# Performance work log

Measured on AMD Instinct MI355X. Metric: run time of the kernel, lower is better.

## Reference

```python
import jax, jax.numpy as jnp
import numpy as np

N = 50000
E = 800000
D = 96
BN_EPS = 1e-3


def setup_inputs() -> dict:
    key = jax.random.key(0)
    ks = jax.random.split(key, 8)
    inp = {
        "x": jax.random.normal(ks[0], (N, D), dtype=jnp.float32),
        "edge_src": jax.random.randint(ks[1], (E,), 0, N, dtype=jnp.int32),
        "edge_dst": jax.random.randint(ks[2], (E,), 0, N, dtype=jnp.int32),
        "edge_w": jax.random.uniform(ks[3], (E,), dtype=jnp.float32),
        "w1": jax.random.normal(ks[4], (D, D), dtype=jnp.float32) * (1.0 / np.sqrt(D)),
        "w2": jax.random.normal(ks[5], (D, D), dtype=jnp.float32) * (1.0 / np.sqrt(D)),
        "w3": jax.random.normal(ks[6], (D, D), dtype=jnp.float32) * (1.0 / np.sqrt(D)),
    }
    for i in (1, 2, 3):
        inp[f"g{i}"] = jnp.ones((D,), jnp.float32)
        inp[f"b{i}"] = jnp.zeros((D,), jnp.float32)
        inp[f"m{i}"] = jnp.zeros((D,), jnp.float32)
        inp[f"v{i}"] = jnp.ones((D,), jnp.float32)
    return inp


def _gcn(x, w, edge_src, edge_dst, edge_w):
    # GraphConvolution: h = x @ W; out = relu(adj @ h)  (sparse COO spmm)
    h = x @ w                                        # [N, D]
    msg = edge_w[:, None] * h[edge_src]              # [E, D]
    agg = jax.ops.segment_sum(msg, edge_dst, num_segments=N)  # [N, D]
    return jax.nn.relu(agg)


def _bn(x, gamma, beta, mean, var):
    # keras BatchNormalization, inference mode, eps=1e-3
    return (x - mean) * (gamma * jax.lax.rsqrt(var + BN_EPS)) + beta


def reference(x, edge_src, edge_dst, edge_w,
              w1, w2, w3,
              g1, b1, m1, v1,
              g2, b2, m2, v2,
              g3, b3, m3, v3):
    residual = x
    h = _bn(_gcn(x, w1, edge_src, edge_dst, edge_w), g1, b1, m1, v1)
    h = _bn(_gcn(h, w2, edge_src, edge_dst, edge_w), g2, b2, m2, v2)
    h = _bn(_gcn(h, w3, edge_src, edge_dst, edge_w), g3, b3, m3, v3)
    return h + residual
```

## Files before the change

kernel.cpp:

```cpp
#include <hip/hip_runtime.h>
#include <hip/hip_fp16.h>

#define DF 96
#define BN_EPS 1e-3f
#define MAXNB 1024
#define PTILE 2048
#define HTILE 2048

template<bool FUSE_BN, bool HALF_IN, bool HALF_OUT>
__global__ __launch_bounds__(192) void gemm_bn_kernel(
    const void* __restrict__ Ain, const float* __restrict__ W,
    const float* __restrict__ g, const float* __restrict__ b,
    const float* __restrict__ m, const float* __restrict__ v,
    void* __restrict__ Cout, int N)
{
    __shared__ __half2 sWh[96 * 48];
    __shared__ float   sA[64 * 100];
    __shared__ float   sS[96], sT[96];

    const int tid  = threadIdx.x;
    const int row0 = blockIdx.x * 64;

    if (FUSE_BN && tid < 96) {
        float s = g[tid] * rsqrtf(v[tid] + BN_EPS);
        sS[tid] = s;
        sT[tid] = b[tid] - m[tid] * s;
    }
    {
        const float4* Wv = reinterpret_cast<const float4*>(W);
        #pragma unroll
        for (int i = 0; i < 12; ++i) {
            int f = tid + 192 * i;
            float4 w = Wv[f];
            sWh[2 * f]     = __floats2half2_rn(w.x, w.y);
            sWh[2 * f + 1] = __floats2half2_rn(w.z, w.w);
        }
    }
    __syncthreads();

    #pragma unroll
    for (int i = 0; i < 8; ++i) {
        int f   = tid + 192 * i;
        int row = f / 24;
        int cc  = (f % 24) * 4;
        int gr  = row0 + row;
        float4 val = make_float4(0.f, 0.f, 0.f, 0.f);
        if (gr < N) {
            if (HALF_IN) {
                const __half* Ah = (const __half*)Ain + (size_t)gr * DF + cc;
                float2 raw = *reinterpret_cast<const float2*>(Ah);
                union { float2 f2; __half2 h[2]; } u; u.f2 = raw;
                float2 lo = __half22float2(u.h[0]);
                float2 hi = __half22float2(u.h[1]);
                val = make_float4(lo.x, lo.y, hi.x, hi.y);
            } else {
                val = *reinterpret_cast<const float4*>(
                          (const float*)Ain + (size_t)gr * DF + cc);
            }
            if (FUSE_BN) {
                float* p = &val.x;
                #pragma unroll
                for (int j = 0; j < 4; ++j) {
                    float x_ = p[j];
                    x_ = x_ > 0.f ? x_ : 0.f;
                    p[j] = x_ * sS[cc + j] + sT[cc + j];
                }
            }
        }
        *reinterpret_cast<float4*>(sA + row * 100 + cc) = val;
    }
    __syncthreads();

    const int tx = tid % 24, ty = tid / 24;
    float acc[8][4];
    #pragma unroll
    for (int i = 0; i < 8; ++i)
        for (int j = 0; j < 4; ++j) acc[i][j] = 0.f;

    for (int k = 0; k < 96; ++k) {
        float2 wa = __half22float2(sWh[k * 48 + tx * 2]);
        float2 wb = __half22float2(sWh[k * 48 + tx * 2 + 1]);
        #pragma unroll
        for (int i = 0; i < 8; ++i) {
            float a = sA[(ty + 8 * i) * 100 + k];
            acc[i][0] += a * wa.x;
            acc[i][1] += a * wa.y;
            acc[i][2] += a * wb.x;
            acc[i][3] += a * wb.y;
        }
    }
    const int c0 = tx * 4;
    #pragma unroll
    for (int i = 0; i < 8; ++i) {
        int gr = row0 + ty + 8 * i;
        if (gr >= N) continue;
        if (HALF_OUT) {
            __half* C = (__half*)Cout;
            ushort4 u;
            u.x = __half_as_ushort(__float2half_rn(acc[i][0]));
            u.y = __half_as_ushort(__float2half_rn(acc[i][1]));
            u.z = __half_as_ushort(__float2half_rn(acc[i][2]));
            u.w = __half_as_ushort(__float2half_rn(acc[i][3]));
            *reinterpret_cast<ushort4*>(C + (size_t)gr * DF + c0) = u;
        } else {
            float* C = (float*)Cout;
            *reinterpret_cast<float4*>(C + (size_t)gr * DF + c0) =
                make_float4(acc[i][0], acc[i][1], acc[i][2], acc[i][3]);
        }
    }
}

__global__ void zero_kernel(int* __restrict__ p, int n)
{
    int i = blockIdx.x * blockDim.x + threadIdx.x;
    if (i < n) p[i] = 0;
}

__global__ __launch_bounds__(256) void bucket_hist_kernel(
    const int* __restrict__ dst, int* __restrict__ bcnt, int E, int NB)
{
    __shared__ int lc[MAXNB];
    for (int i = threadIdx.x; i < NB; i += 256) lc[i] = 0;
    __syncthreads();
    int base = blockIdx.x * HTILE;
    #pragma unroll
    for (int j = 0; j < HTILE / 256; ++j) {
        int i = base + j * 256 + threadIdx.x;
        if (i < E) atomicAdd(&lc[dst[i] >> 6], 1);
    }
    __syncthreads();
    for (int i = threadIdx.x; i < NB; i += 256) {
        int c = lc[i];
        if (c) atomicAdd(&bcnt[i], c);
    }
}

__global__ __launch_bounds__(256) void bucket_scan_kernel(
    int* __restrict__ bbase, int* __restrict__ bcur, int NB)
{
    __shared__ int wsum[4];
    int t = threadIdx.x, lane = t & 63, wv = t >> 6;
    int vals[4], s = 0;
    #pragma unroll
    for (int j = 0; j < 4; ++j) {
        int idx = t * 4 + j;
        vals[j] = (idx < NB) ? bcur[idx] : 0;
        s += vals[j];
    }
    int inc = s;
    #pragma unroll
    for (int o = 1; o < 64; o <<= 1) {
        int u = __shfl_up(inc, o);
        if (lane >= o) inc += u;
    }
    int excl = inc - s;
    if (lane == 63) wsum[wv] = inc;
    __syncthreads();
    if (t == 0) {
        int run = 0;
        #pragma unroll
        for (int j = 0; j < 4; ++j) { int vv = wsum[j]; wsum[j] = run; run += vv; }
    }
    __syncthreads();
    int off = wsum[wv] + excl;
    #pragma unroll
    for (int j = 0; j < 4; ++j) {
        int idx = t * 4 + j;
        if (idx < NB) { bbase[idx] = off; bcur[idx] = off; off += vals[j]; }
    }
}

__global__ __launch_bounds__(256) void partition_kernel(
    const int* __restrict__ src, const int* __restrict__ dst,
    const float* __restrict__ ew, int* __restrict__ bcur,
    int2* __restrict__ ebufA, int E, int NB)
{
    __shared__ int lc[MAXNB];
    for (int i = threadIdx.x; i < NB; i += 256) lc[i] = 0;
    __syncthreads();
    int base = blockIdx.x * PTILE;
    #pragma unroll
    for (int j = 0; j < PTILE / 256; ++j) {
        int i = base + j * 256 + threadIdx.x;
        if (i < E) atomicAdd(&lc[dst[i] >> 6], 1);
    }
    __syncthreads();
    for (int i = threadIdx.x; i < NB; i += 256) {
        int c = lc[i];
        lc[i] = c ? atomicAdd(&bcur[i], c) : 0;
    }
    __syncthreads();
    #pragma unroll
    for (int j = 0; j < PTILE / 256; ++j) {
        int i = base + j * 256 + threadIdx.x;
        if (i < E) {
            int d   = dst[i];
            int bkt = d >> 6;
            int pos = atomicAdd(&lc[bkt], 1);
            ebufA[pos] = make_int2(src[i] | ((d & 63) << 26), __float_as_int(ew[i]));
        }
    }
}

__global__ __launch_bounds__(256) void csr_bucket_kernel(
    const int2* __restrict__ ebufA, const int* __restrict__ bbase,
    const int* __restrict__ bcur, int2* __restrict__ pairs,
    int* __restrict__ row_ptr, int N, int E, int NB)
{
    __shared__ int lc[64];
    int t   = threadIdx.x;
    int bkt = blockIdx.x;
    int e0  = bbase[bkt];
    int cnt = bcur[bkt] - e0;

    if (t < 64) lc[t] = 0;
    __syncthreads();
    for (int i = t; i < cnt; i += 256)
        atomicAdd(&lc[((unsigned)ebufA[e0 + i].x) >> 26], 1);
    __syncthreads();
    if (t < 64) {
        int v   = lc[t];
        int inc = v;
        #pragma unroll
        for (int o = 1; o < 64; o <<= 1) {
            int u = __shfl_up(inc, o);
            if (t >= o) inc += u;
        }
        int excl = inc - v;
        int node = (bkt << 6) + t;
        if (node < N) row_ptr[node] = e0 + excl;
        lc[t] = excl;
    }
    __syncthreads();
    for (int i = t; i < cnt; i += 256) {
        int2 p = ebufA[e0 + i];
        unsigned px = (unsigned)p.x;
        int pos = atomicAdd(&lc[px >> 26], 1);
        pairs[e0 + pos] = make_int2((int)(px & 0x03FFFFFFu), p.y);
    }
    if (bkt == NB - 1 && t == 0) row_ptr[N] = E;
}

template<bool FINAL, bool HALF, bool OHALF>
__global__ __launch_bounds__(192) void gather_kernel(
    const void* __restrict__ hbuf, const int2* __restrict__ pairs,
    const int* __restrict__ row_ptr, void* __restrict__ out,
    const float* __restrict__ xres,
    const float* __restrict__ g, const float* __restrict__ b,
    const float* __restrict__ m, const float* __restrict__ v, int N)
{
    __shared__ __attribute__((aligned(16))) float sS[96];
    __shared__ __attribute__((aligned(16))) float sT[96];
    if (FINAL) {
        int t = threadIdx.x;
        if (t < 96) {
            float s = g[t] * rsqrtf(v[t] + BN_EPS);
            sS[t] = s;
            sT[t] = b[t] - m[t] * s;
        }
        __syncthreads();
    }
    int node = blockIdx.x * 8 + threadIdx.x / 24;
    int q    = threadIdx.x % 24;
    if (node >= N) return;

    auto ld = [&](int srcR) -> float4 {
        if (HALF) {
            const __half* hp = (const __half*)hbuf + (size_t)srcR * DF + q * 4;
            float2 raw = *reinterpret_cast<const float2*>(hp);
            union { float2 f; __half2 h[2]; } u; u.f = raw;
            float2 lo = __half22float2(u.h[0]);
            float2 hi = __half22float2(u.h[1]);
            return make_float4(lo.x, lo.y, hi.x, hi.y);
        } else {
            return *(reinterpret_cast<const float4*>(
                        (const float*)hbuf + (size_t)srcR * DF) + q);
        }
    };

    int e   = row_ptr[node];
    int end = row_ptr[node + 1];
    float ax = 0.f, ay = 0.f, az = 0.f, aw = 0.f;

    auto fma1 = [&](int sr, float w) {
        float4 hv = ld(sr);
        ax = fmaf(w, hv.x, ax); ay = fmaf(w, hv.y, ay);
        az = fmaf(w, hv.z, az); aw = fmaf(w, hv.w, aw);
    };

    if (e < end && (e & 1)) {
        int2 p = pairs[e];
        fma1(p.x, __int_as_float(p.y));
        ++e;
    }
    const int4* p2 = reinterpret_cast<const int4*>(pairs);

    for (; e + 8 <= end; e += 8) {
        int h0 = e >> 1;
        int4 q0 = p2[h0 + 0];
        int4 q1 = p2[h0 + 1];
        int4 q2 = p2[h0 + 2];
        int4 q3 = p2[h0 + 3];
        float4 v0 = ld(q0.x), v1 = ld(q0.z);
        float4 v2 = ld(q1.x), v3 = ld(q1.z);
        float4 v4 = ld(q2.x), v5 = ld(q2.z);
        float4 v6 = ld(q3.x), v7 = ld(q3.z);
        float w0 = __int_as_float(q0.y), w1 = __int_as_float(q0.w);
        float w2 = __int_as_float(q1.y), w3 = __int_as_float(q1.w);
        float w4 = __int_as_float(q2.y), w5 = __int_as_float(q2.w);
        float w6 = __int_as_float(q3.y), w7 = __int_as_float(q3.w);
        ax = fmaf(w0, v0.x, ax); ay = fmaf(w0, v0.y, ay);
        az = fmaf(w0, v0.z, az); aw = fmaf(w0, v0.w, aw);
        ax = fmaf(w1, v1.x, ax); ay = fmaf(w1, v1.y, ay);
        az = fmaf(w1, v1.z, az); aw = fmaf(w1, v1.w, aw);
        ax = fmaf(w2, v2.x, ax); ay = fmaf(w2, v2.y, ay);
        az = fmaf(w2, v2.z, az); aw = fmaf(w2, v2.w, aw);
        ax = fmaf(w3, v3.x, ax); ay = fmaf(w3, v3.y, ay);
        az = fmaf(w3, v3.z, az); aw = fmaf(w3, v3.w, aw);
        ax = fmaf(w4, v4.x, ax); ay = fmaf(w4, v4.y, ay);
        az = fmaf(w4, v4.z, az); aw = fmaf(w4, v4.w, aw);
        ax = fmaf(w5, v5.x, ax); ay = fmaf(w5, v5.y, ay);
        az = fmaf(w5, v5.z, az); aw = fmaf(w5, v5.w, aw);
        ax = fmaf(w6, v6.x, ax); ay = fmaf(w6, v6.y, ay);
        az = fmaf(w6, v6.z, az); aw = fmaf(w6, v6.w, aw);
        ax = fmaf(w7, v7.x, ax); ay = fmaf(w7, v7.y, ay);
        az = fmaf(w7, v7.z, az); aw = fmaf(w7, v7.w, aw);
    }
    for (; e + 2 <= end; e += 2) {
        int4 q0 = p2[e >> 1];
        float4 v0 = ld(q0.x), v1 = ld(q0.z);
        float w0 = __int_as_float(q0.y), w1 = __int_as_float(q0.w);
        ax = fmaf(w0, v0.x, ax); ay = fmaf(w0, v0.y, ay);
        az = fmaf(w0, v0.z, az); aw = fmaf(w0, v0.w, aw);
        ax = fmaf(w1, v1.x, ax); ay = fmaf(w1, v1.y, ay);
        az = fmaf(w1, v1.z, az); aw = fmaf(w1, v1.w, aw);
    }
    if (e < end) {
        int2 p = pairs[e];
        fma1(p.x, __int_as_float(p.y));
    }

    size_t o = (size_t)node * DF + q * 4;
    if (FINAL) {
        int c = q * 4;
        float* of = (float*)out;
        float4 xv = *reinterpret_cast<const float4*>(xres + o);
        float4 s4 = *reinterpret_cast<const float4*>(sS + c);
        float4 t4 = *reinterpret_cast<const float4*>(sT + c);
        float4 r;
        r.x = fmaf(fmaxf(ax, 0.f), s4.x, t4.x) + xv.x;
        r.y = fmaf(fmaxf(ay, 0.f), s4.y, t4.y) + xv.y;
        r.z = fmaf(fmaxf(az, 0.f), s4.z, t4.z) + xv.z;
        r.w = fmaf(fmaxf(aw, 0.f), s4.w, t4.w) + xv.w;
        *reinterpret_cast<float4*>(of + o) = r;
    } else if (OHALF) {
        __half* oh = (__half*)out;
        ushort4 u;
        u.x = __half_as_ushort(__float2half_rn(ax));
        u.y = __half_as_ushort(__float2half_rn(ay));
        u.z = __half_as_ushort(__float2half_rn(az));
        u.w = __half_as_ushort(__float2half_rn(aw));
        *reinterpret_cast<ushort4*>(oh + o) = u;
    } else {
        *reinterpret_cast<float4*>((float*)out + o) =
            make_float4(ax, ay, az, aw);
    }
}

__global__ __launch_bounds__(256) void scatter_kernel(
    const float* __restrict__ h, const int* __restrict__ src,
    const int* __restrict__ dst, const float* __restrict__ ew,
    float* __restrict__ agg, int E)
{
    long long t = (long long)blockIdx.x * blockDim.x + threadIdx.x;
    if (t >= (long long)E * 24) return;
    int e  = (int)(t / 24);
    int cc = (int)(t % 24) * 4;
    int s  = src[e];
    int d  = dst[e];
    float w = ew[e];
    float4 hv = *reinterpret_cast<const float4*>(h + (size_t)s * DF + cc);
    float* out = agg + (size_t)d * DF + cc;
    atomicAdd(out + 0, w * hv.x);
    atomicAdd(out + 1, w * hv.y);
    atomicAdd(out + 2, w * hv.z);
    atomicAdd(out + 3, w * hv.w);
}

__global__ __launch_bounds__(256) void final_kernel(
    const float* __restrict__ agg, const float* __restrict__ x,
    const float* __restrict__ g, const float* __restrict__ b,
    const float* __restrict__ m, const float* __restrict__ v,
    float* __restrict__ out, int total4)
{
    int i = blockIdx.x * blockDim.x + threadIdx.x;
    if (i >= total4) return;
    int cc = (i % 24) * 4;
    float4 a4 = reinterpret_cast<const float4*>(agg)[i];
    float4 x4 = reinterpret_cast<const float4*>(x)[i];
    float* pa = &a4.x;
    const float* px = &x4.x;
    float4 o;
    float* po = &o.x;
    #pragma unroll
    for (int j = 0; j < 4; ++j) {
        int c = cc + j;
        float s  = g[c] * rsqrtf(v[c] + BN_EPS);
        float tt = b[c] - m[c] * s;
        float a  = pa[j] > 0.f ? pa[j] : 0.f;
        po[j] = a * s + tt + px[j];
    }
    reinterpret_cast<float4*>(out)[i] = o;
}

extern "C" void kernel_launch(void* const* d_in, const int* in_sizes, int n_in,
                              void* d_out, int out_size, void* d_ws, size_t ws_size,
                              hipStream_t stream)
{
    const float* x    = (const float*)d_in[0];
    const int*   esrc = (const int*)d_in[1];
    const int*   edst = (const int*)d_in[2];
    const float* ew   = (const float*)d_in[3];
    const float* w1   = (const float*)d_in[4];
    const float* w2   = (const float*)d_in[5];
    const float* w3   = (const float*)d_in[6];
    const float* g1 = (const float*)d_in[7],  *b1 = (const float*)d_in[8];
    const float* m1 = (const float*)d_in[9],  *v1 = (const float*)d_in[10];
    const float* g2 = (const float*)d_in[11], *b2 = (const float*)d_in[12];
    const float* m2 = (const float*)d_in[13], *v2 = (const float*)d_in[14];
    const float* g3 = (const float*)d_in[15], *b3 = (const float*)d_in[16];
    const float* m3 = (const float*)d_in[17], *v3 = (const float*)d_in[18];

    const int N  = in_sizes[0] / DF;
    const int E  = in_sizes[1];
    const int NB = (N + 63) >> 6;
    const size_t nbytes = (size_t)N * DF * sizeof(float);
    const size_t hh_bytes = (size_t)N * DF * 2;

    float* B = (float*)d_out;

    auto up = [](size_t s) { return (s + 255) & ~(size_t)255; };
    size_t off_agg   = 0;
    size_t off_pairs = off_agg   + up(nbytes);
    size_t off_rptr  = off_pairs + up((size_t)E * 8);
    size_t off_bbase = off_rptr  + up(((size_t)N + 1) * 4);
    size_t off_bcur  = off_bbase + up((size_t)NB * 4);
    size_t off_ebufA = off_bcur  + up((size_t)NB * 4);
    size_t need_f32  = off_ebufA + up((size_t)E * 8);
    size_t ovl       = (size_t)E * 8 > hh_bytes ? (size_t)E * 8 : hh_bytes;
    size_t need_f16  = off_ebufA + up(ovl);

    char*  ws = (char*)d_ws;
    float* A  = (float*)(ws + off_agg);

    const int gemm_grid = (N + 63) / 64;
    const bool ok = (NB <= MAXNB) && (N < (1 << 26)) && (ws_size >= need_f32);

    if (ok) {
        int2*   ebufA  = (int2*)(ws + off_ebufA);
        __half* Hh     = (__half*)(ws + off_ebufA);
        __half* Ah     = (__half*)(ws + off_agg);
        int2*   pairs  = (int2*)(ws + off_pairs);
        int*    rowptr = (int*) (ws + off_rptr);
        int*    bbase  = (int*) (ws + off_bbase);
        int*    bcur   = (int*) (ws + off_bcur);
        const bool half_h = (ws_size >= need_f16);

        zero_kernel<<<(NB + 255) / 256, 256, 0, stream>>>(bcur, NB);
        bucket_hist_kernel<<<(E + HTILE - 1) / HTILE, 256, 0, stream>>>(
            edst, bcur, E, NB);
        bucket_scan_kernel<<<1, 256, 0, stream>>>(bbase, bcur, NB);
        partition_kernel<<<(E + PTILE - 1) / PTILE, 256, 0, stream>>>(
            esrc, edst, ew, bcur, ebufA, E, NB);
        csr_bucket_kernel<<<NB, 256, 0, stream>>>(
            ebufA, bbase, bcur, pairs, rowptr, N, E, NB);

        const int ggrid = (N + 7) / 8;

        if (half_h) {
            gemm_bn_kernel<false, false, true><<<gemm_grid, 192, 0, stream>>>(
                x, w1, nullptr, nullptr, nullptr, nullptr, Hh, N);
            gather_kernel<false, true, true><<<ggrid, 192, 0, stream>>>(
                Hh, pairs, rowptr, Ah, nullptr, nullptr, nullptr, nullptr, nullptr, N);
            gemm_bn_kernel<true, true, true><<<gemm_grid, 192, 0, stream>>>(
                Ah, w2, g1, b1, m1, v1, Hh, N);
            gather_kernel<false, true, true><<<ggrid, 192, 0, stream>>>(
                Hh, pairs, rowptr, Ah, nullptr, nullptr, nullptr, nullptr, nullptr, N);
            gemm_bn_kernel<true, true, true><<<gemm_grid, 192, 0, stream>>>(
                Ah, w3, g2, b2, m2, v2, Hh, N);
            gather_kernel<true, true, false><<<ggrid, 192, 0, stream>>>(
                Hh, pairs, rowptr, B, x, g3, b3, m3, v3, N);
        } else {
            gemm_bn_kernel<false, false, false><<<gemm_grid, 192, 0, stream>>>(
                x, w1, nullptr, nullptr, nullptr, nullptr, B, N);
            gather_kernel<false, false, false><<<ggrid, 192, 0, stream>>>(
                B, pairs, rowptr, A, nullptr, nullptr, nullptr, nullptr, nullptr, N);
            gemm_bn_kernel<true, false, false><<<gemm_grid, 192, 0, stream>>>(
                A, w2, g1, b1, m1, v1, B, N);
            gather_kernel<false, false, false><<<ggrid, 192, 0, stream>>>(
                B, pairs, rowptr, A, nullptr, nullptr, nullptr, nullptr, nullptr, N);
            gemm_bn_kernel<true, false, false><<<gemm_grid, 192, 0, stream>>>(
                A, w3, g2, b2, m2, v2, A, N);
            gather_kernel<true, false, false><<<ggrid, 192, 0, stream>>>(
                A, pairs, rowptr, B, x, g3, b3, m3, v3, N);
        }
    } else {
        const long long st     = (long long)E * 24;
        const int scatter_grid = (int)((st + 255) / 256);
        const int total4       = N * 24;
        const int final_grid   = (total4 + 255) / 256;

        hipMemsetAsync(A, 0, nbytes, stream);
        gemm_bn_kernel<false, false, false><<<gemm_grid, 192, 0, stream>>>(
            x, w1, nullptr, nullptr, nullptr, nullptr, B, N);
        scatter_kernel<<<scatter_grid, 256, 0, stream>>>(B, esrc, edst, ew, A, E);

        gemm_bn_kernel<true, false, false><<<gemm_grid, 192, 0, stream>>>(
            A, w2, g1, b1, m1, v1, B, N);
        hipMemsetAsync(A, 0, nbytes, stream);
        scatter_kernel<<<scatter_grid, 256, 0, stream>>>(B, esrc, edst, ew, A, E);

        gemm_bn_kernel<true, false, false><<<gemm_grid, 192, 0, stream>>>(
            A, w3, g2, b2, m2, v2, B, N);
        hipMemsetAsync(A, 0, nbytes, stream);
        scatter_kernel<<<scatter_grid, 256, 0, stream>>>(B, esrc, edst, ew, A, E);

        final_kernel<<<final_grid, 256, 0, stream>>>(
            A, x, g3, b3, m3, v3, (float*)d_out, total4);
    }
}
```

Before: 217.1 us.

## Fuse gather aggregation with next-layer GEMM and BN into one kernel

Adds a kernel that gathers neighbor rows for 8 nodes per block, applies ReLU and the batch-norm affine, stages the result in shared memory, and multiplies by a half-precision copy of the next weight matrix held in shared memory. It replaces the separate gather and GEMM launches for layers 2 and 3, so the intermediate aggregate is no longer written to and re-read from global memory. The cost is loading the full 96x96 weight matrix into shared memory for every 8-node block, a small GEMM tile with low reuse, and a small added kernel that converts the weights to half.

```diff
diff --git a/kernel.cpp b/kernel.cpp
--- a/kernel.cpp
+++ b/kernel.cpp
@@ -114,6 +114,17 @@
 {
     int i = blockIdx.x * blockDim.x + threadIdx.x;
     if (i < n) p[i] = 0;
+}
+
+__global__ void convw_kernel(const float* __restrict__ w2,
+                             const float* __restrict__ w3,
+                             __half* __restrict__ o2, __half* __restrict__ o3)
+{
+    int i = blockIdx.x * blockDim.x + threadIdx.x;
+    if (i < 96 * 96) {
+        o2[i] = __float2half_rn(w2[i]);
+        o3[i] = __float2half_rn(w3[i]);
+    }
 }
 
 __global__ __launch_bounds__(256) void bucket_hist_kernel(
@@ -367,6 +378,135 @@
     }
 }
 
+__global__ __launch_bounds__(192) void fused_gather_gemm_kernel(
+    const __half* __restrict__ hin, const int2* __restrict__ pairs,
+    const int* __restrict__ row_ptr, const __half* __restrict__ Wh,
+    const float* __restrict__ g, const float* __restrict__ b,
+    const float* __restrict__ m, const float* __restrict__ v,
+    __half* __restrict__ hout, int N)
+{
+    __shared__ __half2 sWh[96 * 48];
+    __shared__ float   sRow[8][100];
+    __shared__ float   sS[96], sT[96];
+
+    const int t = threadIdx.x;
+    if (t < 96) {
+        float s = g[t] * rsqrtf(v[t] + BN_EPS);
+        sS[t] = s;
+        sT[t] = b[t] - m[t] * s;
+    }
+    {
+        const uint4* srcw = reinterpret_cast<const uint4*>(Wh);
+        uint4*       dstw = reinterpret_cast<uint4*>(sWh);
+        #pragma unroll
+        for (int i = 0; i < 6; ++i) dstw[t + 192 * i] = srcw[t + 192 * i];
+    }
+
+    const int  node  = t / 24;
+    const int  q     = t % 24;
+    const int  nodeg = blockIdx.x * 8 + node;
+    const bool valid = nodeg < N;
+
+    float ax = 0.f, ay = 0.f, az = 0.f, aw = 0.f;
+    if (valid) {
+        auto ld = [&](int srcR) -> float4 {
+            const __half* hp = hin + (size_t)srcR * DF + q * 4;
+            float2 raw = *reinterpret_cast<const float2*>(hp);
+            union { float2 f; __half2 h[2]; } u; u.f = raw;
+            float2 lo = __half22float2(u.h[0]);
+            float2 hi = __half22float2(u.h[1]);
+            return make_float4(lo.x, lo.y, hi.x, hi.y);
+        };
+        int e   = row_ptr[nodeg];
+        int end = row_ptr[nodeg + 1];
+        if (e < end && (e & 1)) {
+            int2 p = pairs[e];
+            float4 hv = ld(p.x);
+            float w = __int_as_float(p.y);
+            ax = fmaf(w, hv.x, ax); ay = fmaf(w, hv.y, ay);
+            az = fmaf(w, hv.z, az); aw = fmaf(w, hv.w, aw);
+            ++e;
+        }
+        const int4* p2 = reinterpret_cast<const int4*>(pairs);
+        for (; e + 8 <= end; e += 8) {
+            int h0 = e >> 1;
+            int4 q0 = p2[h0 + 0];
+            int4 q1 = p2[h0 + 1];
+            int4 q2 = p2[h0 + 2];
+            int4 q3 = p2[h0 + 3];
+            float4 v0 = ld(q0.x), v1 = ld(q0.z);
+            float4 v2 = ld(q1.x), v3 = ld(q1.z);
+            float4 v4 = ld(q2.x), v5 = ld(q2.z);
+            float4 v6 = ld(q3.x), v7 = ld(q3.z);
+            float w0 = __int_as_float(q0.y), w1 = __int_as_float(q0.w);
+            float w2 = __int_as_float(q1.y), w3 = __int_as_float(q1.w);
+            float w4 = __int_as_float(q2.y), w5 = __int_as_float(q2.w);
+            float w6 = __int_as_float(q3.y), w7 = __int_as_float(q3.w);
+            ax = fmaf(w0, v0.x, ax); ay = fmaf(w0, v0.y, ay);
+            az = fmaf(w0, v0.z, az); aw = fmaf(w0, v0.w, aw);
+            ax = fmaf(w1, v1.x, ax); ay = fmaf(w1, v1.y, ay);
+            az = fmaf(w1, v1.z, az); aw = fmaf(w1, v1.w, aw);
+            ax = fmaf(w2, v2.x, ax); ay = fmaf(w2, v2.y, ay);
+            az = fmaf(w2, v2.z, az); aw = fmaf(w2, v2.w, aw);
+            ax = fmaf(w3, v3.x, ax); ay = fmaf(w3, v3.y, ay);
+            az = fmaf(w3, v3.z, az); aw = fmaf(w3, v3.w, aw);
+            ax = fmaf(w4, v4.x, ax); ay = fmaf(w4, v4.y, ay);
+            az = fmaf(w4, v4.z, az); aw = fmaf(w4, v4.w, aw);
+            ax = fmaf(w5, v5.x, ax); ay = fmaf(w5, v5.y, ay);
+            az = fmaf(w5, v5.z, az); aw = fmaf(w5, v5.w, aw);
+            ax = fmaf(w6, v6.x, ax); ay = fmaf(w6, v6.y, ay);
+            az = fmaf(w6, v6.z, az); aw = fmaf(w6, v6.w, aw);
+            ax = fmaf(w7, v7.x, ax); ay = fmaf(w7, v7.y, ay);
+            az = fmaf(w7, v7.z, az); aw = fmaf(w7, v7.w, aw);
+        }
+        for (; e + 2 <= end; e += 2) {
+            int4 q0 = p2[e >> 1];
+            float4 v0 = ld(q0.x), v1 = ld(q0.z);
+            float w0 = __int_as_float(q0.y), w1 = __int_as_float(q0.w);
+            ax = fmaf(w0, v0.x, ax); ay = fmaf(w0, v0.y, ay);
+            az = fmaf(w0, v0.z, az); aw = fmaf(w0, v0.w, aw);
+            ax = fmaf(w1, v1.x, ax); ay = fmaf(w1, v1.y, ay);
+            az = fmaf(w1, v1.z, az); aw = fmaf(w1, v1.w, aw);
+        }
+        if (e < end) {
+            int2 p = pairs[e];
+            float4 hv = ld(p.x);
+            float w = __int_as_float(p.y);
+            ax = fmaf(w, hv.x, ax); ay = fmaf(w, hv.y, ay);
+            az = fmaf(w, hv.z, az); aw = fmaf(w, hv.w, aw);
+        }
+    }
+    __syncthreads();
+
+    if (valid) {
+        int c = q * 4;
+        sRow[node][c + 0] = fmaf(fmaxf(ax, 0.f), sS[c + 0], sT[c + 0]);
+        sRow[node][c + 1] = fmaf(fmaxf(ay, 0.f), sS[c + 1], sT[c + 1]);
+        sRow[node][c + 2] = fmaf(fmaxf(az, 0.f), sS[c + 2], sT[c + 2]);
+        sRow[node][c + 3] = fmaf(fmaxf(aw, 0.f), sS[c + 3], sT[c + 3]);
+    }
+    __syncthreads();
+
+    float o0 = 0.f, o1 = 0.f, o2 = 0.f, o3 = 0.f;
+    for (int k = 0; k < 96; ++k) {
+        float2 wa = __half22float2(sWh[k * 48 + q * 2]);
+        float2 wb = __half22float2(sWh[k * 48 + q * 2 + 1]);
+        float a = sRow[node][k];
+        o0 = fmaf(a, wa.x, o0);
+        o1 = fmaf(a, wa.y, o1);
+        o2 = fmaf(a, wb.x, o2);
+        o3 = fmaf(a, wb.y, o3);
+    }
+    if (valid) {
+        ushort4 u;
+        u.x = __half_as_ushort(__float2half_rn(o0));
+        u.y = __half_as_ushort(__float2half_rn(o1));
+        u.z = __half_as_ushort(__float2half_rn(o2));
+        u.w = __half_as_ushort(__float2half_rn(o3));
+        *reinterpret_cast<ushort4*>(hout + (size_t)nodeg * DF + q * 4) = u;
+    }
+}
+
 __global__ __launch_bounds__(256) void scatter_kernel(
     const float* __restrict__ h, const int* __restrict__ src,
     const int* __restrict__ dst, const float* __restrict__ ew,
@@ -436,6 +576,7 @@
     const int NB = (N + 63) >> 6;
     const size_t nbytes = (size_t)N * DF * sizeof(float);
     const size_t hh_bytes = (size_t)N * DF * 2;
+    const size_t wh_bytes = (size_t)96 * 96 * 2;
 
     float* B = (float*)d_out;
 
@@ -445,7 +586,9 @@
     size_t off_rptr  = off_pairs + up((size_t)E * 8);
     size_t off_bbase = off_rptr  + up(((size_t)N + 1) * 4);
     size_t off_bcur  = off_bbase + up((size_t)NB * 4);
-    size_t off_ebufA = off_bcur  + up((size_t)NB * 4);
+    size_t off_wh2   = off_bcur  + up((size_t)NB * 4);
+    size_t off_wh3   = off_wh2   + up(wh_bytes);
+    size_t off_ebufA = off_wh3   + up(wh_bytes);
     size_t need_f32  = off_ebufA + up((size_t)E * 8);
     size_t ovl       = (size_t)E * 8 > hh_bytes ? (size_t)E * 8 : hh_bytes;
     size_t need_f16  = off_ebufA + up(ovl);
@@ -458,8 +601,10 @@
 
     if (ok) {
         int2*   ebufA  = (int2*)(ws + off_ebufA);
-        __half* Hh     = (__half*)(ws + off_ebufA);
-        __half* Ah     = (__half*)(ws + off_agg);
+        __half* HhA    = (__half*)(ws + off_ebufA);
+        __half* HhB    = (__half*)(ws + off_agg);
+        __half* Wh2    = (__half*)(ws + off_wh2);
+        __half* Wh3    = (__half*)(ws + off_wh3);
         int2*   pairs  = (int2*)(ws + off_pairs);
         int*    rowptr = (int*) (ws + off_rptr);
         int*    bbase  = (int*) (ws + off_bbase);
@@ -478,18 +623,16 @@
         const int ggrid = (N + 7) / 8;
 
         if (half_h) {
+            convw_kernel<<<(96 * 96 + 255) / 256, 256, 0, stream>>>(
+                w2, w3, Wh2, Wh3);
             gemm_bn_kernel<false, false, true><<<gemm_grid, 192, 0, stream>>>(
-                x, w1, nullptr, nullptr, nullptr, nullptr, Hh, N);
-            gather_kernel<false, true, true><<<ggrid, 192, 0, stream>>>(
-                Hh, pairs, rowptr, Ah, nullptr, nullptr, nullptr, nullptr, nullptr, N);
-            gemm_bn_kernel<true, true, true><<<gemm_grid, 192, 0, stream>>>(
-                Ah, w2, g1, b1, m1, v1, Hh, N);
-            gather_kernel<false, true, true><<<ggrid, 192, 0, stream>>>(
-                Hh, pairs, rowptr, Ah, nullptr, nullptr, nullptr, nullptr, nullptr, N);
-            gemm_bn_kernel<true, true, true><<<gemm_grid, 192, 0, stream>>>(
-                Ah, w3, g2, b2, m2, v2, Hh, N);
+                x, w1, nullptr, nullptr, nullptr, nullptr, HhA, N);
+            fused_gather_gemm_kernel<<<ggrid, 192, 0, stream>>>(
+                HhA, pairs, rowptr, Wh2, g1, b1, m1, v1, HhB, N);
+            fused_gather_gemm_kernel<<<ggrid, 192, 0, stream>>>(
+                HhB, pairs, rowptr, Wh3, g2, b2, m2, v2, HhA, N);
             gather_kernel<true, true, false><<<ggrid, 192, 0, stream>>>(
-                Hh, pairs, rowptr, B, x, g3, b3, m3, v3, N);
+                HhA, pairs, rowptr, B, x, g3, b3, m3, v3, N);
         } else {
             gemm_bn_kernel<false, false, false><<<gemm_grid, 192, 0, stream>>>(
                 x, w1, nullptr, nullptr, nullptr, nullptr, B, N);
```

New measurement: 200.9 us. 1.08x faster.
